# Kernel tuning notes

Measured on AMD Instinct MI355X. Metric: run time of the kernel, lower is better.

The kernel has to match this reference:

```python
import jax, jax.numpy as jnp
import numpy as np

B, T, IN, H, NL = 64, 256, 64, 768, 2
LU, OUT = 256, 1
INPUT_SCALE = 1.5
OUTPUT_SCALE = 70.0
STD = 0.001  # nn.init.normal_(p, std=0.001) on all LSTM params


def setup_inputs() -> dict:
    key = jax.random.key(0)
    ks = jax.random.split(key, 16)
    inp = {"x": jax.random.normal(ks[0], (B, T, IN), jnp.float32)}
    dims = [IN, H]
    for l in range(NL):
        d = dims[l]
        inp[f"Wih{l}"] = (jax.random.normal(ks[1 + 4 * l], (4 * H, d)) * STD).astype(jnp.float32)
        inp[f"Whh{l}"] = (jax.random.normal(ks[2 + 4 * l], (4 * H, H)) * STD).astype(jnp.float32)
        inp[f"bih{l}"] = (jax.random.normal(ks[3 + 4 * l], (4 * H,)) * STD).astype(jnp.float32)
        inp[f"bhh{l}"] = (jax.random.normal(ks[4 + 4 * l], (4 * H,)) * STD).astype(jnp.float32)
    # MLP head (torch default-ish small init)
    inp["W1"] = (jax.random.normal(ks[9], (LU, H)) * (1.0 / np.sqrt(H))).astype(jnp.float32)
    inp["b1"] = jnp.zeros((LU,), jnp.float32)
    inp["W2"] = (jax.random.normal(ks[10], (OUT, LU)) * (1.0 / np.sqrt(LU))).astype(jnp.float32)
    inp["b2"] = jnp.zeros((OUT,), jnp.float32)
    return inp


def _lstm_layer(x, Wih, Whh, bih, bhh):
    # x: (B, T, D) -> hidden sequence (B, T, H). PyTorch gate order: i, f, g, o.
    b = x.shape[0]
    h = Whh.shape[1]
    # precompute input contributions for all timesteps: (B, T, 4H)
    xg = jnp.einsum('btd,gd->btg', x, Wih) + bih + bhh

    def step(carry, xt):
        hp, cp = carry
        gates = xt + hp @ Whh.T  # (B, 4H)
        i, f, g, o = jnp.split(gates, 4, axis=-1)
        c = jax.nn.sigmoid(f) * cp + jax.nn.sigmoid(i) * jnp.tanh(g)
        hn = jax.nn.sigmoid(o) * jnp.tanh(c)
        return (hn, c), hn

    h0 = jnp.zeros((b, h), x.dtype)
    (_, _), hs = jax.lax.scan(step, (h0, h0), xg.transpose(1, 0, 2))
    return hs.transpose(1, 0, 2)  # (B, T, H)


def reference(x, Wih0, Whh0, bih0, bhh0, Wih1, Whh1, bih1, bhh1, W1, b1, W2, b2):
    xs = x / INPUT_SCALE
    h1 = _lstm_layer(xs, Wih0, Whh0, bih0, bhh0)
    h2 = _lstm_layer(h1, Wih1, Whh1, bih1, bhh1)
    last = h2[:, -1, :]                       # (B, H)
    z = jax.nn.soft_sign(last @ W1.T + b1)    # Softsign: x / (1 + |x|)
    pred = (z @ W2.T + b2) * OUTPUT_SCALE     # (B, OUT)
    return pred[:, None, :]                   # unsqueeze(1) -> (B, 1, OUT)
```

## Files before the change

kernel.cpp:

```cpp
#include <hip/hip_runtime.h>
#include <hip/hip_bf16.h>


#define B_  64
#define T_  256
#define IN_ 64
#define H_  768
#define G_  3072
#define K0_ 832
#define K1_ 1536
#define NWG0 96
#define NWGC 192
#define NWGT 256
#define CB_  96
#define SLOT_ (CB_ * 64 * 8)

typedef __bf16 bf16_t;
typedef bf16_t bf16x8 __attribute__((ext_vector_type(8)));
typedef float  f32x4  __attribute__((ext_vector_type(4)));

__device__ __forceinline__ unsigned short f2bf(float f) {
    union { float f; unsigned u; } v; v.f = f;
    unsigned r = v.u + 0x7FFFu + ((v.u >> 16) & 1u);
    return (unsigned short)(r >> 16);
}
__device__ __forceinline__ float fast_sigm(float x) {
    float e = __builtin_amdgcn_exp2f(-1.44269504f * x);
    return __builtin_amdgcn_rcpf(1.0f + e);
}
__device__ __forceinline__ float fast_tanh(float x) {
    float e = __builtin_amdgcn_exp2f(2.88539008f * x);
    return (e - 1.0f) * __builtin_amdgcn_rcpf(e + 1.0f);
}
__device__ __forceinline__ void st_llc_u32(unsigned* p, unsigned v) {
    asm volatile("global_store_dword %0, %1, off sc1" :: "v"(p), "v"(v) : "memory");
}
#define MFMA16(a, b, c) __builtin_amdgcn_mfma_f32_16x16x32_bf16((a), (b), (c), 0, 0, 0)
#define AGENT_LD(p) __hip_atomic_load((p), __ATOMIC_RELAXED, __HIP_MEMORY_SCOPE_AGENT)

__global__ __launch_bounds__(256) void prep_kernel(
    const float* __restrict__ x,
    const float* __restrict__ Wih0, const float* __restrict__ Whh0,
    const float* __restrict__ bih0, const float* __restrict__ bhh0,
    const float* __restrict__ Wih1, const float* __restrict__ Whh1,
    const float* __restrict__ bih1, const float* __restrict__ bhh1,
    unsigned short* __restrict__ xsT,
    unsigned short* __restrict__ W0cat,
    unsigned short* __restrict__ W1cat,
    float* __restrict__ bias0, float* __restrict__ bias1,
    int* __restrict__ ctrs)
{
    int i = blockIdx.x * blockDim.x + threadIdx.x;
    int stride = gridDim.x * blockDim.x;
    for (int j = i; j < B_ * T_ * IN_; j += stride) {
        int b = j >> 14;
        int t = (j >> 6) & (T_ - 1);
        int k = j & (IN_ - 1);
        xsT[(((size_t)t * B_) + b) * IN_ + k] = f2bf(x[j] * (1.0f / 1.5f));
    }
    for (int j = i; j < G_ * IN_; j += stride) {
        int r = j >> 6; int k = j & 63;
        W0cat[(size_t)r * K0_ + k] = f2bf(Wih0[j]);
    }
    for (int j = i; j < G_ * H_; j += stride) {
        int r = j / H_; int k = j - r * H_;
        W0cat[(size_t)r * K0_ + IN_ + k] = f2bf(Whh0[j]);
        W1cat[(size_t)r * K1_ + k]       = f2bf(Wih1[j]);
        W1cat[(size_t)r * K1_ + H_ + k]  = f2bf(Whh1[j]);
    }
    for (int j = i; j < G_; j += stride) {
        bias0[j] = bih0[j] + bhh0[j];
        bias1[j] = bih1[j] + bhh1[j];
    }
    for (int j = i; j < 2048; j += stride) ctrs[j] = 0;
}

__global__ __launch_bounds__(256) void lstm_persistent(
    const unsigned short* __restrict__ xsT,
    const unsigned short* __restrict__ W0cat,
    const unsigned short* __restrict__ W1cat,
    const float* __restrict__ bias0, const float* __restrict__ bias1,
    unsigned short* __restrict__ h1ring,
    unsigned short* __restrict__ h2ring,
    float* __restrict__ hf32,
    int* __restrict__ ctrs)
{
    __shared__ unsigned short ldsb[4][16][8];

    const int tid  = threadIdx.x;
    const int lane = tid & 63;
    const int wave = tid >> 6;
    const int wg   = blockIdx.x;

    if (wg >= NWGC) {
        int* done = &ctrs[1536];
        float a = 1.0f + (float)tid * 1e-7f;
        const float bm = 1.0000001f, cm = 1e-9f;
        for (;;) {
            for (int i = 0; i < 2048; i++)
                a = __builtin_fmaf(a, bm, cm);
            asm volatile("" : "+v"(a));
            int d = 0;
            if (lane == 0) d = AGENT_LD(done);
            d = __builtin_amdgcn_readfirstlane(d);
            if (d != 0) break;
        }
        return;
    }

    const bool isL1 = (wg >= NWG0);
    const int cb   = isL1 ? (wg - NWG0) : wg;
    const int c0   = cb * 8;
    const int frow = lane & 15;
    const int q    = lane >> 4;
    const int kof  = q * 8;
    const int m0   = wave * 16;

    int* ctr0 = &ctrs[0];
    int* ctr1 = &ctrs[256];

    const unsigned short* Wc = isL1 ? W1cat : W0cat;
    const int Kc = isL1 ? K1_ : K0_;
    int q0 = frow >> 3, col0 = c0 + (frow & 7);
    const unsigned short* Bp0 = Wc + (size_t)(q0 * H_ + col0) * Kc + kof;
    const unsigned short* Bp1 = Wc + (size_t)((2 + q0) * H_ + col0) * Kc + kof;

    const float* bias = isL1 ? bias1 : bias0;
    const bool lowhalf = (lane & 15) < 8;
    const int ecol = c0 + (lane & 7);
    float bi = 0.f, bff = 0.f, bg = 0.f, bo = 0.f;
    if (lowhalf) {
        bi  = bias[0 * H_ + ecol];
        bff = bias[1 * H_ + ecol];
        bg  = bias[2 * H_ + ecol];
        bo  = bias[3 * H_ + ecol];
    }
    float creg[4] = {0.f, 0.f, 0.f, 0.f};

    const size_t aoff = (size_t)q * 512 + (size_t)(m0 + frow) * 8;
    const size_t stoff_e = (size_t)cb * 512 + (size_t)(m0 + (lane >> 2)) * 8
                         + (size_t)(lane & 3) * 2;

    if (!isL1) {
        for (int s = 0; s < T_; ++s) {
            f32x4 acc0 = {0.f, 0.f, 0.f, 0.f};
            f32x4 acc1 = {0.f, 0.f, 0.f, 0.f};
            {
                const unsigned short* xsp =
                    xsT + ((size_t)s * B_ + m0 + frow) * IN_ + kof;
                #pragma unroll
                for (int ki = 0; ki < 2; ki++) {
                    bf16x8 a  = *(const bf16x8*)(xsp + ki * 32);
                    bf16x8 b0 = *(const bf16x8*)(Bp0 + ki * 32);
                    bf16x8 b1 = *(const bf16x8*)(Bp1 + ki * 32);
                    acc0 = MFMA16(a, b0, acc0);
                    acc1 = MFMA16(a, b1, acc1);
                }
            }
            if (s > 0) {
                if (tid == 0) {
                    while (AGENT_LD(ctr0) < NWG0 * s)
                        __builtin_amdgcn_s_sleep(1);
                }
                __syncthreads();
                const unsigned short* hr = h1ring + (size_t)(s - 1) * SLOT_ + aoff;
                #pragma unroll
                for (int kj = 0; kj < 24; kj++) {
                    bf16x8 a  = *(const bf16x8*)(hr + kj * 2048);
                    bf16x8 b0 = *(const bf16x8*)(Bp0 + (kj + 2) * 32);
                    bf16x8 b1 = *(const bf16x8*)(Bp1 + (kj + 2) * 32);
                    acc0 = MFMA16(a, b0, acc0);
                    acc1 = MFMA16(a, b1, acc1);
                }
            }
            f32x4 pacc0, pacc1;
            #pragma unroll
            for (int j = 0; j < 4; j++) {
                pacc0[j] = __shfl_xor(acc0[j], 8);
                pacc1[j] = __shfl_xor(acc1[j], 8);
            }
            if (lowhalf) {
                #pragma unroll
                for (int j = 0; j < 4; j++) {
                    float pi = acc0[j]  + bi;
                    float pf = pacc0[j] + bff;
                    float pg = acc1[j]  + bg;
                    float po = pacc1[j] + bo;
                    float cn = fast_sigm(pf) * creg[j] + fast_sigm(pi) * fast_tanh(pg);
                    float hn = fast_sigm(po) * fast_tanh(cn);
                    creg[j] = cn;
                    ldsb[wave][q * 4 + j][lane & 7] = f2bf(hn);
                }
            }
            unsigned v = ((const unsigned*)&ldsb[wave][0][0])[lane];
            st_llc_u32((unsigned*)(h1ring + (size_t)s * SLOT_ + stoff_e), v);
            __syncthreads();
            if (tid == 0) atomicAdd(ctr0, 1);
        }
    } else {
        for (int s = 1; s <= T_; ++s) {
            const int t = s - 1;
            if (tid == 0) {
                while (AGENT_LD(ctr0) < NWG0 * s)
                    __builtin_amdgcn_s_sleep(1);
            }
            if (tid == 64 && t > 0) {
                while (AGENT_LD(ctr1) < NWG0 * t)
                    __builtin_amdgcn_s_sleep(1);
            }
            __syncthreads();
            f32x4 acc0 = {0.f, 0.f, 0.f, 0.f};
            f32x4 acc1 = {0.f, 0.f, 0.f, 0.f};
            const unsigned short* h1r = h1ring + (size_t)t * SLOT_ + aoff;
            #pragma unroll
            for (int ki = 0; ki < 24; ki++) {
                bf16x8 a  = *(const bf16x8*)(h1r + ki * 2048);
                bf16x8 b0 = *(const bf16x8*)(Bp0 + ki * 32);
                bf16x8 b1 = *(const bf16x8*)(Bp1 + ki * 32);
                acc0 = MFMA16(a, b0, acc0);
                acc1 = MFMA16(a, b1, acc1);
            }
            if (t > 0) {
                const unsigned short* h2r = h2ring + (size_t)(t - 1) * SLOT_ + aoff;
                #pragma unroll
                for (int ki = 0; ki < 24; ki++) {
                    bf16x8 a  = *(const bf16x8*)(h2r + ki * 2048);
                    bf16x8 b0 = *(const bf16x8*)(Bp0 + (ki + 24) * 32);
                    bf16x8 b1 = *(const bf16x8*)(Bp1 + (ki + 24) * 32);
                    acc0 = MFMA16(a, b0, acc0);
                    acc1 = MFMA16(a, b1, acc1);
                }
            }
            f32x4 pacc0, pacc1;
            #pragma unroll
            for (int j = 0; j < 4; j++) {
                pacc0[j] = __shfl_xor(acc0[j], 8);
                pacc1[j] = __shfl_xor(acc1[j], 8);
            }
            if (lowhalf) {
                #pragma unroll
                for (int j = 0; j < 4; j++) {
                    int row = m0 + q * 4 + j;
                    float pi = acc0[j]  + bi;
                    float pf = pacc0[j] + bff;
                    float pg = acc1[j]  + bg;
                    float po = pacc1[j] + bo;
                    float cn = fast_sigm(pf) * creg[j] + fast_sigm(pi) * fast_tanh(pg);
                    float hn = fast_sigm(po) * fast_tanh(cn);
                    creg[j] = cn;
                    ldsb[wave][q * 4 + j][lane & 7] = f2bf(hn);
                    if (t == T_ - 1) hf32[(size_t)row * H_ + ecol] = hn;
                }
            }
            unsigned v = ((const unsigned*)&ldsb[wave][0][0])[lane];
            st_llc_u32((unsigned*)(h2ring + (size_t)t * SLOT_ + stoff_e), v);
            __syncthreads();
            if (tid == 0) atomicAdd(ctr1, 1);
        }
        if (tid == 0) st_llc_u32((unsigned*)&ctrs[1536], 1u);
    }
}

__global__ __launch_bounds__(256) void head_kernel(
    const float* __restrict__ hlast,
    const float* __restrict__ W1, const float* __restrict__ b1,
    const float* __restrict__ W2, const float* __restrict__ b2,
    float* __restrict__ out)
{
    __shared__ float hs[H_];
    __shared__ float partial[4];
    int b = blockIdx.x;
    int tid = threadIdx.x;
    for (int j = tid; j < H_; j += 256) hs[j] = hlast[(size_t)b * H_ + j];
    __syncthreads();
    float z = 0.f;
    const float* w = W1 + (size_t)tid * H_;
    for (int j = 0; j < H_; j++) z += hs[j] * w[j];
    z += b1[tid];
    z = z / (1.0f + fabsf(z));
    float p = z * W2[tid];
    #pragma unroll
    for (int off = 32; off > 0; off >>= 1) p += __shfl_down(p, off, 64);
    if ((tid & 63) == 0) partial[tid >> 6] = p;
    __syncthreads();
    if (tid == 0) {
        float s = partial[0] + partial[1] + partial[2] + partial[3];
        out[b] = (s + b2[0]) * 70.0f;
    }
}

extern "C" void kernel_launch(void* const* d_in, const int* in_sizes, int n_in,
                              void* d_out, int out_size, void* d_ws, size_t ws_size,
                              hipStream_t stream) {
    const float* x    = (const float*)d_in[0];
    const float* Wih0 = (const float*)d_in[1];
    const float* Whh0 = (const float*)d_in[2];
    const float* bih0 = (const float*)d_in[3];
    const float* bhh0 = (const float*)d_in[4];
    const float* Wih1 = (const float*)d_in[5];
    const float* Whh1 = (const float*)d_in[6];
    const float* bih1 = (const float*)d_in[7];
    const float* bhh1 = (const float*)d_in[8];
    const float* W1   = (const float*)d_in[9];
    const float* b1   = (const float*)d_in[10];
    const float* W2   = (const float*)d_in[11];
    const float* b2   = (const float*)d_in[12];
    float* out = (float*)d_out;

    char* w = (char*)d_ws;
    int* ctrs = (int*)w;                          w += 8192;
    unsigned short* h1ring = (unsigned short*)w;  w += (size_t)T_ * SLOT_ * 2;
    unsigned short* h2ring = (unsigned short*)w;  w += (size_t)T_ * SLOT_ * 2;
    unsigned short* xsT    = (unsigned short*)w;  w += (size_t)B_ * T_ * IN_ * 2;
    unsigned short* W0cat  = (unsigned short*)w;  w += (size_t)G_ * K0_ * 2;
    unsigned short* W1cat  = (unsigned short*)w;  w += (size_t)G_ * K1_ * 2;
    float* bias0 = (float*)w;                     w += G_ * 4;
    float* bias1 = (float*)w;                     w += G_ * 4;
    float* hf32  = (float*)w;                     w += (size_t)B_ * H_ * 4;

    prep_kernel<<<1024, 256, 0, stream>>>(x, Wih0, Whh0, bih0, bhh0,
                                          Wih1, Whh1, bih1, bhh1,
                                          xsT, W0cat, W1cat, bias0, bias1, ctrs);
    lstm_persistent<<<NWGT, 256, 0, stream>>>(xsT, W0cat, W1cat, bias0, bias1,
                                              h1ring, h2ring, hf32, ctrs);
    head_kernel<<<B_, 256, 0, stream>>>(hf32, W1, b1, W2, b2, out);
}
```

Baseline: 3.237 ms.

## Replace atomic counter barrier with per-WG flags and aggregator broadcast

Swaps the single atomic counter that every workgroup increments and polls for a per-workgroup flag store. Two dedicated aggregator workgroups, one per layer, poll all 96 flags and broadcast an epoch value to 8 replicated slots, so pollers spread their loads across separate cache lines. This is meant to remove atomic contention and polling hot-spots on one address in the per-timestep grid barrier. The cost is an extra hop through the aggregator on every step, which adds latency to the critical path, and two of the spinner workgroups are repurposed as aggregators.

```diff
diff --git a/kernel.cpp b/kernel.cpp
--- a/kernel.cpp
+++ b/kernel.cpp
@@ -37,6 +37,7 @@
 }
 #define MFMA16(a, b, c) __builtin_amdgcn_mfma_f32_16x16x32_bf16((a), (b), (c), 0, 0, 0)
 #define AGENT_LD(p) __hip_atomic_load((p), __ATOMIC_RELAXED, __HIP_MEMORY_SCOPE_AGENT)
+
 
 __global__ __launch_bounds__(256) void prep_kernel(
     const float* __restrict__ x,
@@ -92,8 +93,32 @@
     const int wave = tid >> 6;
     const int wg   = blockIdx.x;
 
-    if (wg >= NWGC) {
-        int* done = &ctrs[1536];
+    int* flags0 = &ctrs[0];
+    int* flags1 = &ctrs[256];
+    int* ep0    = &ctrs[512];
+    int* ep1    = &ctrs[768];
+    int* done   = &ctrs[1536];
+
+    if (wg == NWGC || wg == NWGC + 1) {
+        if (wave != 0) return;
+        const bool agg1 = (wg == NWGC + 1);
+        int* fl = agg1 ? flags1 : flags0;
+        int* ep = agg1 ? ep1 : ep0;
+        const int i1 = lane;
+        const int i2 = 64 + (lane & 31);
+        for (int e = 1; e <= T_; ++e) {
+            for (;;) {
+                int fa = AGENT_LD(&fl[i1]);
+                int fb = AGENT_LD(&fl[i2]);
+                if (__all(fa >= e && fb >= e)) break;
+                __builtin_amdgcn_s_sleep(1);
+            }
+            if (lane < 8) st_llc_u32((unsigned*)&ep[lane * 16], (unsigned)e);
+        }
+        if (agg1 && lane == 0) st_llc_u32((unsigned*)done, 1u);
+        return;
+    }
+    if (wg > NWGC + 1) {
         float a = 1.0f + (float)tid * 1e-7f;
         const float bm = 1.0000001f, cm = 1e-9f;
         for (;;) {
@@ -116,8 +141,8 @@
     const int kof  = q * 8;
     const int m0   = wave * 16;
 
-    int* ctr0 = &ctrs[0];
-    int* ctr1 = &ctrs[256];
+    int* myrep0 = &ep0[(wg & 7) * 16];
+    int* myrep1 = &ep1[(wg & 7) * 16];
 
     const unsigned short* Wc = isL1 ? W1cat : W0cat;
     const int Kc = isL1 ? K1_ : K0_;
@@ -159,7 +184,7 @@
             }
             if (s > 0) {
                 if (tid == 0) {
-                    while (AGENT_LD(ctr0) < NWG0 * s)
+                    while (AGENT_LD(myrep0) < s)
                         __builtin_amdgcn_s_sleep(1);
                 }
                 __syncthreads();
@@ -195,17 +220,17 @@
             unsigned v = ((const unsigned*)&ldsb[wave][0][0])[lane];
             st_llc_u32((unsigned*)(h1ring + (size_t)s * SLOT_ + stoff_e), v);
             __syncthreads();
-            if (tid == 0) atomicAdd(ctr0, 1);
+            if (tid == 0) st_llc_u32((unsigned*)&flags0[cb], (unsigned)(s + 1));
         }
     } else {
         for (int s = 1; s <= T_; ++s) {
             const int t = s - 1;
             if (tid == 0) {
-                while (AGENT_LD(ctr0) < NWG0 * s)
+                while (AGENT_LD(myrep0) < s)
                     __builtin_amdgcn_s_sleep(1);
             }
             if (tid == 64 && t > 0) {
-                while (AGENT_LD(ctr1) < NWG0 * t)
+                while (AGENT_LD(myrep1) < t)
                     __builtin_amdgcn_s_sleep(1);
             }
             __syncthreads();
@@ -255,9 +280,8 @@
             unsigned v = ((const unsigned*)&ldsb[wave][0][0])[lane];
             st_llc_u32((unsigned*)(h2ring + (size_t)t * SLOT_ + stoff_e), v);
             __syncthreads();
-            if (tid == 0) atomicAdd(ctr1, 1);
+            if (tid == 0) st_llc_u32((unsigned*)&flags1[cb], (unsigned)s);
         }
-        if (tid == 0) st_llc_u32((unsigned*)&ctrs[1536], 1u);
     }
 }
 
```

After: 3.166 ms. -2.2%, faster.
